# Performance work log

Hardware: AMD Instinct MI355X
Metric: run time of the kernel (lower is better)

The kernel has to match this reference:

```python
import jax, jax.numpy as jnp
import numpy as np

B, R, F = 64, 196, 2048   # batch, regions, feature_dim
E, H, A = 512, 512, 512   # embed_dim, hidden_dim, attn_dim
V, L = 12000, 24          # vocab, seq_len


def setup_inputs() -> dict:
    key = jax.random.key(0)
    ks = jax.random.split(key, 16)
    s = lambda *d: 1.0 / np.sqrt(d[-1])
    inp = {
        'image_feats': jax.random.normal(ks[0], (B, R, F), jnp.float32),
        'caption_in': jax.random.randint(ks[1], (B, L), 0, V, jnp.int64),
        'emb_table': jax.random.normal(ks[2], (V, E), jnp.float32) * 0.02,
        'W_init_h': jax.random.normal(ks[3], (H, F), jnp.float32) * s(F),
        'b_init_h': jnp.zeros((H,), jnp.float32),
        'W_init_c': jax.random.normal(ks[4], (H, F), jnp.float32) * s(F),
        'b_init_c': jnp.zeros((H,), jnp.float32),
        'W_ih': jax.random.normal(ks[5], (4 * H, E + F), jnp.float32) * s(E + F),
        'b_ih': jnp.zeros((4 * H,), jnp.float32),
        'W_hh': jax.random.normal(ks[6], (4 * H, H), jnp.float32) * s(H),
        'b_hh': jnp.zeros((4 * H,), jnp.float32),
        'W_featp': jax.random.normal(ks[7], (A, F), jnp.float32) * s(F),
        'b_featp': jnp.zeros((A,), jnp.float32),
        'W_hidp': jax.random.normal(ks[8], (A, H), jnp.float32) * s(H),
        'b_hidp': jnp.zeros((A,), jnp.float32),
        'W_score': jax.random.normal(ks[9], (1, A), jnp.float32) * s(A),
        'b_score': jnp.zeros((1,), jnp.float32),
        'W_out': jax.random.normal(ks[10], (V, H), jnp.float32) * s(H),
        'b_out': jnp.zeros((V,), jnp.float32),
    }
    return inp


def _forward(image_feats, caption_in, emb_table, W_init_h, b_init_h, W_init_c,
             b_init_c, W_ih, b_ih, W_hh, b_hh, W_featp, b_featp, W_hidp,
             b_hidp, W_score, b_score, W_out, b_out):
    # init hidden state from mean image features
    mean_feats = image_feats.mean(axis=1)                      # (B, F)
    h0 = mean_feats @ W_init_h.T + b_init_h                    # (B, H)
    c0 = mean_feats @ W_init_c.T + b_init_c                    # (B, H)

    embeddings = emb_table[caption_in]                         # (B, L, E)  (dropout in eval mode = identity)

    # feature projection is constant over timesteps -> hoist out of the scan
    feat_proj = jnp.einsum('brf,af->bra', image_feats, W_featp) + b_featp  # (B, R, A)

    def step(carry, emb_t):
        h, c = carry
        # additive attention
        hid_proj = h @ W_hidp.T + b_hidp                       # (B, A)
        energy = jnp.tanh(feat_proj + hid_proj[:, None, :])    # (B, R, A)
        scores = jnp.einsum('bra,a->br', energy, W_score[0]) + b_score[0]
        alpha = jax.nn.softmax(scores, axis=1)                 # (B, R)
        context = jnp.einsum('br,brf->bf', alpha, image_feats) # (B, F)
        # LSTM cell (PyTorch gate order: i, f, g, o)
        x = jnp.concatenate([emb_t, context], axis=1)          # (B, E+F)
        gates = x @ W_ih.T + b_ih + h @ W_hh.T + b_hh          # (B, 4H)
        i, f, g, o = jnp.split(gates, 4, axis=1)
        c_new = jax.nn.sigmoid(f) * c + jax.nn.sigmoid(i) * jnp.tanh(g)
        h_new = jax.nn.sigmoid(o) * jnp.tanh(c_new)
        out = h_new @ W_out.T + b_out                          # (B, V)
        return (h_new, c_new), (out, alpha)

    emb_t = jnp.swapaxes(embeddings, 0, 1)                     # (L, B, E)
    _, (preds, alphas) = jax.lax.scan(step, (h0, c0), emb_t)
    predictions = jnp.swapaxes(preds, 0, 1)                    # (B, L, V)
    all_alphas = jnp.swapaxes(alphas, 0, 1)                    # (B, L, R)
    return predictions, all_alphas


def reference(image_feats, caption_in, emb_table, W_init_h, b_init_h, W_init_c,
              b_init_c, W_ih, b_ih, W_hh, b_hh, W_featp, b_featp, W_hidp,
              b_hidp, W_score, b_score, W_out, b_out):
    return _forward(image_feats, caption_in, emb_table, W_init_h, b_init_h,
                    W_init_c, b_init_c, W_ih, b_ih, W_hh, b_hh, W_featp,
                    b_featp, W_hidp, b_hidp, W_score, b_score, W_out, b_out)
```

## Files before the change

kernel.cpp:

```cpp
#include <hip/hip_runtime.h>

#define B_ 64
#define R_ 196
#define F_ 2048
#define E_ 512
#define H_ 512
#define A_ 512
#define V_ 12000
#define L_ 24

typedef __attribute__((ext_vector_type(8))) short bf16x8;
typedef __attribute__((ext_vector_type(4))) float f32x4;
typedef unsigned short ush;

__device__ __forceinline__ float fast_tanh(float x) {
    float t = __expf(2.f * x);
    return 1.f - 2.f / (t + 1.f);
}
__device__ __forceinline__ float fast_sig(float x) {
    return 1.f / (1.f + __expf(-x));
}
__device__ __forceinline__ ush f2bf(float x) {
    unsigned int u = __float_as_uint(x);
    return (ush)((u + 0x7fffu + ((u >> 16) & 1u)) >> 16);
}
__device__ __forceinline__ float bf2f(ush b) {
    return __uint_as_float(((unsigned int)b) << 16);
}

#define LROW 40

template<int SPLIT, int CMAP, bool NFAST>
__global__ __launch_bounds__(512) void gemm_big128(
    const ush* __restrict__ Ah, const ush* __restrict__ Al, int lda,
    const ush* __restrict__ Wh, const ush* __restrict__ Wl, int ldw,
    const float* __restrict__ bias, void* __restrict__ Cv,
    int ldc, int N, int K)
{
    constexpr int SMEM_BYTES = (SPLIT == 3) ? 61440 : 30720;
    __shared__ __align__(16) char smem[SMEM_BYTES];
    ush* sAh = (ush*)smem;
    ush* sBh = (ush*)(smem + 10240);
    ush* sAl = (ush*)(smem + 30720);
    ush* sBl = (ush*)(smem + 40960);

    const int tid = threadIdx.x;
    const int lane = tid & 63, w = tid >> 6;
    const int mw = w >> 2, nw = w & 3;

    const int nbx = gridDim.x, nby = gridDim.y;
    const int nwg = nbx * nby;
    const int orig = blockIdx.x + nbx * blockIdx.y;
    const int q = nwg >> 3, r = nwg & 7;
    const int xcd = orig & 7, idx = orig >> 3;
    const int lin = (xcd < r ? xcd * (q + 1) : r * (q + 1) + (xcd - r) * q) + idx;
    int bx, by;
    if constexpr (NFAST) { by = lin % nby; bx = lin / nby; }
    else                 { bx = lin % nbx; by = lin / nbx; }
    const int mtile = bx * 128;
    const int ntile = by * 256;

    const int fr = lane & 15, kg = (lane >> 4) * 8;
    const int arow = tid >> 2, aq = (tid & 3) * 8;

    f32x4 acc[4][4];
    #pragma unroll
    for (int mf = 0; mf < 4; ++mf)
        #pragma unroll
        for (int nf = 0; nf < 4; ++nf) acc[mf][nf] = {0.f, 0.f, 0.f, 0.f};

    const uint4 zv = make_uint4(0u, 0u, 0u, 0u);

    for (int kb = 0; kb < K; kb += 32) {
        uint4 a_h = *(const uint4*)(Ah + (size_t)(mtile + arow) * lda + kb + aq);
        uint4 a_l;
        uint4 b_h[2], b_l[2];
        #pragma unroll
        for (int p = 0; p < 2; ++p) {
            const int row = ntile + arow + 128 * p;
            b_h[p] = (row < N) ? *(const uint4*)(Wh + (size_t)row * ldw + kb + aq) : zv;
        }
        if constexpr (SPLIT == 3) {
            a_l = *(const uint4*)(Al + (size_t)(mtile + arow) * lda + kb + aq);
            #pragma unroll
            for (int p = 0; p < 2; ++p) {
                const int row = ntile + arow + 128 * p;
                b_l[p] = (row < N) ? *(const uint4*)(Wl + (size_t)row * ldw + kb + aq) : zv;
            }
        }

        __syncthreads();
        *(uint4*)(sAh + arow * LROW + aq) = a_h;
        #pragma unroll
        for (int p = 0; p < 2; ++p)
            *(uint4*)(sBh + (arow + 128 * p) * LROW + aq) = b_h[p];
        if constexpr (SPLIT == 3) {
            *(uint4*)(sAl + arow * LROW + aq) = a_l;
            #pragma unroll
            for (int p = 0; p < 2; ++p)
                *(uint4*)(sBl + (arow + 128 * p) * LROW + aq) = b_l[p];
        }
        __syncthreads();

        bf16x8 bh[4], bl[4];
        #pragma unroll
        for (int nf = 0; nf < 4; ++nf) {
            bh[nf] = *(const bf16x8*)(sBh + (nw * 64 + nf * 16 + fr) * LROW + kg);
            if constexpr (SPLIT == 3)
                bl[nf] = *(const bf16x8*)(sBl + (nw * 64 + nf * 16 + fr) * LROW + kg);
        }
        #pragma unroll
        for (int mf = 0; mf < 4; ++mf) {
            const bf16x8 ah = *(const bf16x8*)(sAh + (mw * 64 + mf * 16 + fr) * LROW + kg);
            if constexpr (SPLIT == 3) {
                const bf16x8 al = *(const bf16x8*)(sAl + (mw * 64 + mf * 16 + fr) * LROW + kg);
                #pragma unroll
                for (int nf = 0; nf < 4; ++nf) {
                    acc[mf][nf] = __builtin_amdgcn_mfma_f32_16x16x32_bf16(ah, bh[nf], acc[mf][nf], 0, 0, 0);
                    acc[mf][nf] = __builtin_amdgcn_mfma_f32_16x16x32_bf16(ah, bl[nf], acc[mf][nf], 0, 0, 0);
                    acc[mf][nf] = __builtin_amdgcn_mfma_f32_16x16x32_bf16(al, bh[nf], acc[mf][nf], 0, 0, 0);
                }
            } else {
                #pragma unroll
                for (int nf = 0; nf < 4; ++nf)
                    acc[mf][nf] = __builtin_amdgcn_mfma_f32_16x16x32_bf16(ah, bh[nf], acc[mf][nf], 0, 0, 0);
            }
        }
    }

    #pragma unroll
    for (int nf = 0; nf < 4; ++nf) {
        const int nn = ntile + nw * 64 + nf * 16 + fr;
        if (nn < N) {
            const float bv = bias ? bias[nn] : 0.f;
            #pragma unroll
            for (int mf = 0; mf < 4; ++mf) {
                #pragma unroll
                for (int rr = 0; rr < 4; ++rr) {
                    const int m = mtile + mw * 64 + mf * 16 + (lane >> 4) * 4 + rr;
                    const float v = acc[mf][nf][rr] + bv;
                    if constexpr (CMAP == 1)
                        ((ush*)Cv)[(size_t)m * ldc + nn] = f2bf(v);
                    else if constexpr (CMAP == 2) {
                        float* dst = (float*)Cv + (size_t)(m & 63) * (L_ * V_)
                                   + (size_t)(m >> 6) * V_ + nn;
                        __builtin_nontemporal_store(v, dst);
                    } else
                        ((float*)Cv)[(size_t)m * ldc + nn] = v;
                }
            }
        }
    }
}

template<int SPLIT, int CMAP, bool NFAST>
__global__ __launch_bounds__(256) void gemm_big(
    const ush* __restrict__ Ah, const ush* __restrict__ Al, int lda,
    const ush* __restrict__ Wh, const ush* __restrict__ Wl, int ldw,
    const float* __restrict__ bias, void* __restrict__ Cv,
    int ldc, int N, int K)
{
    constexpr int SMEM_BYTES = (SPLIT == 3) ? 51200 : 25600;
    __shared__ __align__(16) char smem[SMEM_BYTES];
    ush* sAh = (ush*)smem;
    ush* sBh = (ush*)(smem + 5120);
    ush* sAl = (ush*)(smem + 25600);
    ush* sBl = (ush*)(smem + 30720);

    const int tid = threadIdx.x;
    const int lane = tid & 63, w = tid >> 6;

    const int nbx = gridDim.x, nby = gridDim.y;
    const int nwg = nbx * nby;
    int lin = blockIdx.x + nbx * blockIdx.y;
    if ((nwg & 7) == 0) {
        const int q = nwg >> 3;
        lin = (lin & 7) * q + (lin >> 3);
    }
    int bx, by;
    if constexpr (NFAST) { by = lin % nby; bx = lin / nby; }
    else                 { bx = lin % nbx; by = lin / nbx; }
    const int mtile = bx * 64;
    const int ntile = by * 256;

    const int fr = lane & 15, kg = (lane >> 4) * 8;
    const int arow = tid >> 2, aq = (tid & 3) * 8;

    f32x4 acc[4][4];
    #pragma unroll
    for (int mf = 0; mf < 4; ++mf)
        #pragma unroll
        for (int nf = 0; nf < 4; ++nf) acc[mf][nf] = {0.f, 0.f, 0.f, 0.f};

    const uint4 zv = make_uint4(0u, 0u, 0u, 0u);

    for (int kb = 0; kb < K; kb += 32) {
        uint4 a_h = *(const uint4*)(Ah + (size_t)(mtile + arow) * lda + kb + aq);
        uint4 a_l;
        uint4 b_h[4], b_l[4];
        #pragma unroll
        for (int p = 0; p < 4; ++p) {
            const int row = ntile + arow + 64 * p;
            b_h[p] = (row < N) ? *(const uint4*)(Wh + (size_t)row * ldw + kb + aq) : zv;
        }
        if constexpr (SPLIT == 3) {
            a_l = *(const uint4*)(Al + (size_t)(mtile + arow) * lda + kb + aq);
            #pragma unroll
            for (int p = 0; p < 4; ++p) {
                const int row = ntile + arow + 64 * p;
                b_l[p] = (row < N) ? *(const uint4*)(Wl + (size_t)row * ldw + kb + aq) : zv;
            }
        }

        __syncthreads();
        *(uint4*)(sAh + arow * LROW + aq) = a_h;
        #pragma unroll
        for (int p = 0; p < 4; ++p)
            *(uint4*)(sBh + (arow + 64 * p) * LROW + aq) = b_h[p];
        if constexpr (SPLIT == 3) {
            *(uint4*)(sAl + arow * LROW + aq) = a_l;
            #pragma unroll
            for (int p = 0; p < 4; ++p)
                *(uint4*)(sBl + (arow + 64 * p) * LROW + aq) = b_l[p];
        }
        __syncthreads();

        bf16x8 bh[4], bl[4];
        #pragma unroll
        for (int nf = 0; nf < 4; ++nf) {
            bh[nf] = *(const bf16x8*)(sBh + (w * 64 + nf * 16 + fr) * LROW + kg);
            if constexpr (SPLIT == 3)
                bl[nf] = *(const bf16x8*)(sBl + (w * 64 + nf * 16 + fr) * LROW + kg);
        }
        #pragma unroll
        for (int mf = 0; mf < 4; ++mf) {
            const bf16x8 ah = *(const bf16x8*)(sAh + (mf * 16 + fr) * LROW + kg);
            if constexpr (SPLIT == 3) {
                const bf16x8 al = *(const bf16x8*)(sAl + (mf * 16 + fr) * LROW + kg);
                #pragma unroll
                for (int nf = 0; nf < 4; ++nf) {
                    acc[mf][nf] = __builtin_amdgcn_mfma_f32_16x16x32_bf16(ah, bh[nf], acc[mf][nf], 0, 0, 0);
                    acc[mf][nf] = __builtin_amdgcn_mfma_f32_16x16x32_bf16(ah, bl[nf], acc[mf][nf], 0, 0, 0);
                    acc[mf][nf] = __builtin_amdgcn_mfma_f32_16x16x32_bf16(al, bh[nf], acc[mf][nf], 0, 0, 0);
                }
            } else {
                #pragma unroll
                for (int nf = 0; nf < 4; ++nf)
                    acc[mf][nf] = __builtin_amdgcn_mfma_f32_16x16x32_bf16(ah, bh[nf], acc[mf][nf], 0, 0, 0);
            }
        }
    }

    #pragma unroll
    for (int nf = 0; nf < 4; ++nf) {
        const int nn = ntile + w * 64 + nf * 16 + fr;
        if (nn < N) {
            const float bv = bias ? bias[nn] : 0.f;
            #pragma unroll
            for (int mf = 0; mf < 4; ++mf) {
                #pragma unroll
                for (int rr = 0; rr < 4; ++rr) {
                    const int m = mtile + mf * 16 + (lane >> 4) * 4 + rr;
                    const float v = acc[mf][nf][rr] + bv;
                    if constexpr (CMAP == 1)
                        ((ush*)Cv)[(size_t)m * ldc + nn] = f2bf(v);
                    else
                        ((float*)Cv)[(size_t)m * ldc + nn] = v;
                }
            }
        }
    }
}

__global__ __launch_bounds__(256) void gemm_gates(
    const ush* __restrict__ Ah0, const ush* __restrict__ Al0, int lda0, int k0,
    const ush* __restrict__ Ah1, const ush* __restrict__ Al1, int lda1,
    const ush* __restrict__ Wh, const ush* __restrict__ Wl, int ldw,
    float* __restrict__ C, int ldc, long zstride, int kChunk)
{
    __shared__ ush sAh[64 * LROW];
    __shared__ ush sBh[64 * LROW];
    __shared__ ush sAl[64 * LROW];
    __shared__ ush sBl[64 * LROW];

    const int tid = threadIdx.x;
    const int ntile = blockIdx.x * 64;
    const int kStart = blockIdx.z * kChunk;
    const int lane = tid & 63, w = tid >> 6;
    const int lrow = tid >> 2;
    const int lcol = (tid & 3) * 8;
    const int nrow = ntile + lrow;

    f32x4 acc[4];
    #pragma unroll
    for (int f = 0; f < 4; ++f) acc[f] = {0.f, 0.f, 0.f, 0.f};

    const int fr = lane & 15;
    const int kg = (lane >> 4) * 8;

    for (int kb = kStart; kb < kStart + kChunk; kb += 32) {
        const ush *ph, *pl; int lda, loc;
        if (kb < k0) { ph = Ah0; pl = Al0; lda = lda0; loc = kb; }
        else         { ph = Ah1; pl = Al1; lda = lda1; loc = kb - k0; }

        uint4 a_h = *(const uint4*)(ph + (size_t)lrow * lda + loc + lcol);
        uint4 b_h = *(const uint4*)(Wh + (size_t)nrow * ldw + kb + lcol);
        uint4 a_l = *(const uint4*)(pl + (size_t)lrow * lda + loc + lcol);
        uint4 b_l = *(const uint4*)(Wl + (size_t)nrow * ldw + kb + lcol);

        __syncthreads();
        *(uint4*)(sAh + lrow * LROW + lcol) = a_h;
        *(uint4*)(sBh + lrow * LROW + lcol) = b_h;
        *(uint4*)(sAl + lrow * LROW + lcol) = a_l;
        *(uint4*)(sBl + lrow * LROW + lcol) = b_l;
        __syncthreads();

        const bf16x8 bh = *(const bf16x8*)(sBh + (16 * w + fr) * LROW + kg);
        const bf16x8 bl = *(const bf16x8*)(sBl + (16 * w + fr) * LROW + kg);

        #pragma unroll
        for (int f = 0; f < 4; ++f) {
            const bf16x8 ah = *(const bf16x8*)(sAh + (16 * f + fr) * LROW + kg);
            const bf16x8 al = *(const bf16x8*)(sAl + (16 * f + fr) * LROW + kg);
            acc[f] = __builtin_amdgcn_mfma_f32_16x16x32_bf16(ah, bh, acc[f], 0, 0, 0);
            acc[f] = __builtin_amdgcn_mfma_f32_16x16x32_bf16(ah, bl, acc[f], 0, 0, 0);
            acc[f] = __builtin_amdgcn_mfma_f32_16x16x32_bf16(al, bh, acc[f], 0, 0, 0);
        }
    }

    const int n = ntile + 16 * w + (lane & 15);
    float* Cz = C + (size_t)blockIdx.z * zstride;
    #pragma unroll
    for (int f = 0; f < 4; ++f)
        #pragma unroll
        for (int rr = 0; rr < 4; ++rr) {
            const int m = 16 * f + (lane >> 4) * 4 + rr;
            Cz[(size_t)m * ldc + n] = acc[f][rr];
        }
}

__global__ __launch_bounds__(256) void prep_feats(
    const float* __restrict__ feats, ush* __restrict__ fbh,
    ush* __restrict__ mh, ush* __restrict__ ml)
{
    const int fs = blockIdx.x;
    const int b  = blockIdx.y;
    const int f = fs * 512 + threadIdx.x * 2;
    const float2* fp = (const float2*)(feats + (size_t)b * R_ * F_ + f);
    ush* fo = fbh + (size_t)b * R_ * F_ + f;
    float sx = 0.f, sy = 0.f;
    for (int r = 0; r < R_; ++r) {
        const float2 v = fp[(size_t)r * (F_ / 2)];
        sx += v.x; sy += v.y;
        ushort2 u; u.x = f2bf(v.x); u.y = f2bf(v.y);
        *(ushort2*)(fo + (size_t)r * F_) = u;
    }
    const float s = 1.f / (float)R_;
    sx *= s; sy *= s;
    const size_t mi = (size_t)b * F_ + f;
    const ush hx = f2bf(sx); mh[mi] = hx;     ml[mi] = f2bf(sx - bf2f(hx));
    const ush hy = f2bf(sy); mh[mi + 1] = hy; ml[mi + 1] = f2bf(sy - bf2f(hy));
}

__global__ __launch_bounds__(256) void gather_split(
    const float* __restrict__ emb, const int* __restrict__ cap,
    ush* __restrict__ eh, ush* __restrict__ el)
{
    const int idx = blockIdx.x * 256 + threadIdx.x;
    const int bt = idx >> 7, j = idx & 127;
    const int tok = cap[bt];
    const float4 v = reinterpret_cast<const float4*>(emb)[(size_t)tok * (E_ / 4) + j];
    const float a[4] = {v.x, v.y, v.z, v.w};
    #pragma unroll
    for (int c = 0; c < 4; ++c) {
        const ush hi = f2bf(a[c]);
        eh[idx * 4 + c] = hi;
        el[idx * 4 + c] = f2bf(a[c] - bf2f(hi));
    }
}

__global__ __launch_bounds__(256) void split_kernel(
    const float* __restrict__ in, ush* __restrict__ hi, ush* __restrict__ lo, int n4)
{
    for (int i = blockIdx.x * 256 + threadIdx.x; i < n4; i += gridDim.x * 256) {
        const float4 v = reinterpret_cast<const float4*>(in)[i];
        const float a[4] = {v.x, v.y, v.z, v.w};
        #pragma unroll
        for (int c = 0; c < 4; ++c) {
            const ush h = f2bf(a[c]);
            hi[i * 4 + c] = h;
            if (lo) lo[i * 4 + c] = f2bf(a[c] - bf2f(h));
        }
    }
}

__global__ __launch_bounds__(256) void prep_wih(
    const float* __restrict__ W_ih, const float* __restrict__ W_hh,
    ush* __restrict__ wxh, ush* __restrict__ wxl,
    ush* __restrict__ wg2h, ush* __restrict__ wg2l)
{
    const int nrow = blockIdx.x;
    for (int k = threadIdx.x; k < E_; k += 256) {
        const float v = W_ih[(size_t)nrow * (E_ + F_) + k];
        const ush h = f2bf(v);
        wxh[(size_t)nrow * E_ + k] = h;
        wxl[(size_t)nrow * E_ + k] = f2bf(v - bf2f(h));
    }
    for (int k = threadIdx.x; k < F_ + H_; k += 256) {
        const float v = (k < F_) ? W_ih[(size_t)nrow * (E_ + F_) + E_ + k]
                                 : W_hh[(size_t)nrow * H_ + (k - F_)];
        const ush h = f2bf(v);
        wg2h[(size_t)nrow * (F_ + H_) + k] = h;
        wg2l[(size_t)nrow * (F_ + H_) + k] = f2bf(v - bf2f(h));
    }
}

__global__ __launch_bounds__(256) void transpose512(
    const float* __restrict__ in, float* __restrict__ out)
{
    const int idx = blockIdx.x * 256 + threadIdx.x;
    const int k = idx >> 9, a = idx & 511;
    out[idx] = in[(size_t)a * 512 + k];
    (void)k;
}

__global__ __launch_bounds__(256) void init_reduce(
    const float* __restrict__ initp, const float* __restrict__ b_init_h,
    const float* __restrict__ b_init_c, float* __restrict__ h0f,
    float* __restrict__ c, ush* __restrict__ h_hi, ush* __restrict__ h_lo)
{
    const int idx = blockIdx.x * 256 + threadIdx.x;
    const int b = idx >> 10, n = idx & 1023;
    float s = 0.f;
    #pragma unroll
    for (int z = 0; z < 8; ++z)
        s += initp[(size_t)z * (B_ * 1024) + (size_t)b * 1024 + n];
    if (n < 512) {
        s += b_init_h[n];
        h0f[b * H_ + n] = s;
        const ush hi = f2bf(s);
        h_hi[b * H_ + n] = hi;
        h_lo[b * H_ + n] = f2bf(s - bf2f(hi));
    } else {
        s += b_init_c[n - 512];
        c[b * H_ + (n - 512)] = s;
    }
}

template<bool ATT>
__global__ __launch_bounds__(512) void step_kernel(
    const float* __restrict__ gparts, const float* __restrict__ egates,
    const float* __restrict__ b_ih, const float* __restrict__ b_hh,
    float* __restrict__ c, const float* __restrict__ h0f,
    ush* __restrict__ h_hi, ush* __restrict__ h_lo,
    ush* __restrict__ hall_hi, ush* __restrict__ hall_lo,
    const float* __restrict__ whpT, const float* __restrict__ b_hidp,
    const ush* __restrict__ fpb, const float* __restrict__ W_score,
    const float* __restrict__ b_score,
    float* __restrict__ alpha, float* __restrict__ alph_out, int t)
{
    __shared__ float sh_h[H_];
    __shared__ float sh_hp[A_];
    __shared__ float sh_ws[A_];
    __shared__ float sh_sc[200];
    __shared__ float red[2];
    const int tid = threadIdx.x;
    const int b = blockIdx.x;
    const int n = tid;

    float hh;
    if (t > 0) {
        const float* eg = egates + ((size_t)b * L_ + (t - 1)) * 2048;
        float gi = b_ih[n] + b_hh[n] + eg[n];
        float gf = b_ih[n + 512] + b_hh[n + 512] + eg[n + 512];
        float gg = b_ih[n + 1024] + b_hh[n + 1024] + eg[n + 1024];
        float go = b_ih[n + 1536] + b_hh[n + 1536] + eg[n + 1536];
        #pragma unroll
        for (int z = 0; z < 8; ++z) {
            const float* gz = gparts + (size_t)z * B_ * 2048 + (size_t)b * 2048;
            gi += gz[n]; gf += gz[n + 512]; gg += gz[n + 1024]; go += gz[n + 1536];
        }
        const float cc = fast_sig(gf) * c[b * H_ + n] + fast_sig(gi) * fast_tanh(gg);
        hh = fast_sig(go) * fast_tanh(cc);
        c[b * H_ + n] = cc;
        const ush hi = f2bf(hh);
        const ush lo = f2bf(hh - bf2f(hi));
        h_hi[b * H_ + n] = hi;
        h_lo[b * H_ + n] = lo;
        const size_t hidx = ((size_t)(t - 1) * B_ + b) * H_ + n;
        hall_hi[hidx] = hi;
        hall_lo[hidx] = lo;
    } else {
        hh = h0f[b * H_ + n];
    }
    if constexpr (!ATT) return;

    sh_h[n] = hh;
    sh_ws[n] = W_score[n];
    __syncthreads();

    {
        float a0 = 0.f, a1 = 0.f, a2 = 0.f, a3 = 0.f;
        #pragma unroll 4
        for (int k = 0; k < H_; k += 4) {
            a0 = fmaf(sh_h[k + 0], whpT[(size_t)(k + 0) * A_ + tid], a0);
            a1 = fmaf(sh_h[k + 1], whpT[(size_t)(k + 1) * A_ + tid], a1);
            a2 = fmaf(sh_h[k + 2], whpT[(size_t)(k + 2) * A_ + tid], a2);
            a3 = fmaf(sh_h[k + 3], whpT[(size_t)(k + 3) * A_ + tid], a3);
        }
        sh_hp[tid] = (a0 + a1) + (a2 + a3) + b_hidp[tid];
    }
    __syncthreads();

    const int lane = tid & 63, wid = tid >> 6;
    for (int r = wid; r < R_; r += 8) {
        const ushort2* row = reinterpret_cast<const ushort2*>(fpb + ((size_t)b * R_ + r) * A_);
        float acc = 0.f;
        #pragma unroll
        for (int j = 0; j < 4; ++j) {
            const ushort2 u = row[lane + 64 * j];
            const int a = 2 * (lane + 64 * j);
            acc += fast_tanh(bf2f(u.x) + sh_hp[a]) * sh_ws[a];
            acc += fast_tanh(bf2f(u.y) + sh_hp[a + 1]) * sh_ws[a + 1];
        }
        for (int off = 32; off > 0; off >>= 1) acc += __shfl_down(acc, off);
        if (lane == 0) sh_sc[r] = acc + b_score[0];
    }
    __syncthreads();

    if (tid < 64) {
        float m = -1e30f;
        for (int r = tid; r < R_; r += 64) m = fmaxf(m, sh_sc[r]);
        for (int off = 32; off > 0; off >>= 1) m = fmaxf(m, __shfl_xor(m, off));
        float s = 0.f;
        for (int r = tid; r < R_; r += 64) s += __expf(sh_sc[r] - m);
        for (int off = 32; off > 0; off >>= 1) s += __shfl_xor(s, off);
        if (tid == 0) { red[0] = m; red[1] = 1.f / s; }
    }
    __syncthreads();
    const float m = red[0], is = red[1];
    if (tid < R_) {
        const float av = __expf(sh_sc[tid] - m) * is;
        alpha[b * R_ + tid] = av;
        alph_out[((size_t)b * L_ + t) * R_ + tid] = av;
    }
}

__global__ __launch_bounds__(256) void ctx_kernel(
    const ush* __restrict__ fbh, const float* __restrict__ alpha,
    ush* __restrict__ ctx_hi, ush* __restrict__ ctx_lo)
{
    __shared__ float sa[R_];
    const int tid = threadIdx.x;
    const int fs = blockIdx.x;
    const int b = blockIdx.y;
    if (tid < R_) sa[tid] = alpha[b * R_ + tid];
    __syncthreads();

    const int f0 = fs * 512 + tid * 2;
    const ush* fp = fbh + (size_t)b * R_ * F_ + f0;
    float cx = 0.f, cy = 0.f;
    #pragma unroll 4
    for (int r = 0; r < R_; ++r) {
        const float a = sa[r];
        const ushort2 u = *(const ushort2*)(fp + (size_t)r * F_);
        cx = fmaf(a, bf2f(u.x), cx); cy = fmaf(a, bf2f(u.y), cy);
    }
    const size_t ci = (size_t)b * F_ + f0;
    const ush hx = f2bf(cx);
    ctx_hi[ci] = hx; ctx_lo[ci] = f2bf(cx - bf2f(hx));
    const ush hy = f2bf(cy);
    ctx_hi[ci + 1] = hy; ctx_lo[ci + 1] = f2bf(cy - bf2f(hy));
}

extern "C" void kernel_launch(void* const* d_in, const int* in_sizes, int n_in,
                              void* d_out, int out_size, void* d_ws, size_t ws_size,
                              hipStream_t stream)
{
    const float* feats    = (const float*)d_in[0];
    const int*   cap      = (const int*)  d_in[1];
    const float* emb      = (const float*)d_in[2];
    const float* W_init_h = (const float*)d_in[3];
    const float* b_init_h = (const float*)d_in[4];
    const float* W_init_c = (const float*)d_in[5];
    const float* b_init_c = (const float*)d_in[6];
    const float* W_ih     = (const float*)d_in[7];
    const float* b_ih     = (const float*)d_in[8];
    const float* W_hh     = (const float*)d_in[9];
    const float* b_hh     = (const float*)d_in[10];
    const float* W_featp  = (const float*)d_in[11];
    const float* b_featp  = (const float*)d_in[12];
    const float* W_hidp   = (const float*)d_in[13];
    const float* b_hidp   = (const float*)d_in[14];
    const float* W_score  = (const float*)d_in[15];
    const float* b_score  = (const float*)d_in[16];
    const float* W_out    = (const float*)d_in[17];
    const float* b_out    = (const float*)d_in[18];

    float* pred     = (float*)d_out;
    float* alph_out = pred + (size_t)B_ * L_ * V_;

    char* p = (char*)d_ws;
    auto alloc = [&](size_t bytes) { char* q = p; p += (bytes + 255) & ~(size_t)255; return q; };

    ush*   fpb    = (ush*)  alloc((size_t)B_ * R_ * A_ * 2);
    ush*   eh     = (ush*)  alloc((size_t)B_ * L_ * E_ * 2);
    ush*   el     = (ush*)  alloc((size_t)B_ * L_ * E_ * 2);
    ush*   mh     = (ush*)  alloc((size_t)B_ * F_ * 2);
    ush*   ml     = (ush*)  alloc((size_t)B_ * F_ * 2);
    ush*   fbh    = (ush*)  alloc((size_t)B_ * R_ * F_ * 2);
    ush*   wfp_h  = (ush*)  alloc((size_t)A_ * F_ * 2);
    ush*   wiH    = (ush*)  alloc((size_t)1024 * F_ * 2);
    ush*   wiL    = (ush*)  alloc((size_t)1024 * F_ * 2);
    ush*   wxh    = (ush*)  alloc((size_t)2048 * E_ * 2);
    ush*   wxl    = (ush*)  alloc((size_t)2048 * E_ * 2);
    ush*   wg2h   = (ush*)  alloc((size_t)2048 * (F_ + H_) * 2);
    ush*   wg2l   = (ush*)  alloc((size_t)2048 * (F_ + H_) * 2);
    ush*   woh    = (ush*)  alloc((size_t)V_ * H_ * 2);
    ush*   wol    = (ush*)  alloc((size_t)V_ * H_ * 2);
    float* whpT   = (float*)alloc((size_t)H_ * A_ * 4);
    float* egates = (float*)alloc((size_t)B_ * L_ * 2048 * 4);
    float* h0f    = (float*)alloc((size_t)B_ * H_ * 4);
    float* c      = (float*)alloc((size_t)B_ * H_ * 4);
    ush*   h_hi   = (ush*)  alloc((size_t)B_ * H_ * 2);
    ush*   h_lo   = (ush*)  alloc((size_t)B_ * H_ * 2);
    ush*   hallh  = (ush*)  alloc((size_t)L_ * B_ * H_ * 2);
    ush*   halll  = (ush*)  alloc((size_t)L_ * B_ * H_ * 2);
    ush*   ctx_hi = (ush*)  alloc((size_t)B_ * F_ * 2);
    ush*   ctx_lo = (ush*)  alloc((size_t)B_ * F_ * 2);
    float* alpha  = (float*)alloc((size_t)B_ * R_ * 4);
    float* gparts = (float*)alloc((size_t)8 * B_ * 2048 * 4);
    float* initp  = (float*)alloc((size_t)8 * B_ * 1024 * 4);

    prep_feats<<<dim3(4, B_), 256, 0, stream>>>(feats, fbh, mh, ml);
    gather_split<<<768, 256, 0, stream>>>(emb, cap, eh, el);
    split_kernel<<<2048, 256, 0, stream>>>(W_out, woh, wol, V_ * H_ / 4);
    split_kernel<<<512, 256, 0, stream>>>(W_init_h, wiH, wiL, H_ * F_ / 4);
    split_kernel<<<512, 256, 0, stream>>>(W_init_c, wiH + (size_t)512 * F_,
                                          wiL + (size_t)512 * F_, H_ * F_ / 4);
    split_kernel<<<512, 256, 0, stream>>>(W_featp, wfp_h, nullptr, A_ * F_ / 4);
    prep_wih<<<2048, 256, 0, stream>>>(W_ih, W_hh, wxh, wxl, wg2h, wg2l);
    transpose512<<<1024, 256, 0, stream>>>(W_hidp, whpT);

    gemm_gates<<<dim3(16, 1, 8), 256, 0, stream>>>(
        mh, ml, F_, F_,
        mh, ml, F_,
        wiH, wiL, F_,
        initp, 1024, (long)B_ * 1024, F_ / 8);
    init_reduce<<<256, 256, 0, stream>>>(initp, b_init_h, b_init_c, h0f, c, h_hi, h_lo);

    gemm_big128<1, 1, true><<<dim3(98, 2), 512, 0, stream>>>(
        fbh, nullptr, F_, wfp_h, nullptr, F_, b_featp, fpb, A_, A_, F_);

    gemm_big<3, 0, false><<<dim3(24, 8), 256, 0, stream>>>(
        eh, el, E_, wxh, wxl, E_, nullptr, egates, 2048, 2048, E_);

    for (int t = 0; t < L_; ++t) {
        step_kernel<true><<<B_, 512, 0, stream>>>(
            gparts, egates, b_ih, b_hh, c, h0f, h_hi, h_lo, hallh, halll,
            whpT, b_hidp, fpb, W_score, b_score, alpha, alph_out, t);

        ctx_kernel<<<dim3(4, B_), 256, 0, stream>>>(fbh, alpha, ctx_hi, ctx_lo);

        gemm_gates<<<dim3(32, 1, 8), 256, 0, stream>>>(
            ctx_hi, ctx_lo, F_, F_,
            h_hi, h_lo, H_,
            wg2h, wg2l, F_ + H_,
            gparts, 4 * H_, (long)B_ * 4 * H_, (F_ + H_) / 8);
    }

    step_kernel<false><<<B_, 512, 0, stream>>>(
        gparts, egates, b_ih, b_hh, c, h0f, h_hi, h_lo, hallh, halll,
        whpT, b_hidp, fpb, W_score, b_score, alpha, alph_out, L_);

    gemm_big128<3, 2, false><<<dim3(12, 47), 512, 0, stream>>>(
        hallh, halll, H_, woh, wol, H_, b_out, pred, 0, V_, H_);
}
```

Before: 2.046 ms.

## Fuse attention context reduction into step kernel and retile feature projection

```diff
diff --git a/kernel.cpp b/kernel.cpp
--- a/kernel.cpp
+++ b/kernel.cpp
@@ -456,8 +456,9 @@
     ush* __restrict__ hall_hi, ush* __restrict__ hall_lo,
     const float* __restrict__ whpT, const float* __restrict__ b_hidp,
     const ush* __restrict__ fpb, const float* __restrict__ W_score,
-    const float* __restrict__ b_score,
-    float* __restrict__ alpha, float* __restrict__ alph_out, int t)
+    const float* __restrict__ b_score, const ush* __restrict__ fbh,
+    ush* __restrict__ ctx_hi, ush* __restrict__ ctx_lo,
+    float* __restrict__ alph_out, int t)
 {
     __shared__ float sh_h[H_];
     __shared__ float sh_hp[A_];
@@ -541,36 +542,33 @@
     const float m = red[0], is = red[1];
     if (tid < R_) {
         const float av = __expf(sh_sc[tid] - m) * is;
-        alpha[b * R_ + tid] = av;
+        sh_sc[tid] = av;
         alph_out[((size_t)b * L_ + t) * R_ + tid] = av;
     }
-}
-
-__global__ __launch_bounds__(256) void ctx_kernel(
-    const ush* __restrict__ fbh, const float* __restrict__ alpha,
-    ush* __restrict__ ctx_hi, ush* __restrict__ ctx_lo)
-{
-    __shared__ float sa[R_];
-    const int tid = threadIdx.x;
-    const int fs = blockIdx.x;
-    const int b = blockIdx.y;
-    if (tid < R_) sa[tid] = alpha[b * R_ + tid];
     __syncthreads();
 
-    const int f0 = fs * 512 + tid * 2;
-    const ush* fp = fbh + (size_t)b * R_ * F_ + f0;
-    float cx = 0.f, cy = 0.f;
-    #pragma unroll 4
-    for (int r = 0; r < R_; ++r) {
-        const float a = sa[r];
-        const ushort2 u = *(const ushort2*)(fp + (size_t)r * F_);
-        cx = fmaf(a, bf2f(u.x), cx); cy = fmaf(a, bf2f(u.y), cy);
-    }
-    const size_t ci = (size_t)b * F_ + f0;
-    const ush hx = f2bf(cx);
-    ctx_hi[ci] = hx; ctx_lo[ci] = f2bf(cx - bf2f(hx));
-    const ush hy = f2bf(cy);
-    ctx_hi[ci + 1] = hy; ctx_lo[ci + 1] = f2bf(cy - bf2f(hy));
+    {
+        const int f0 = tid << 2;
+        const ush* fp2 = fbh + (size_t)b * R_ * F_ + f0;
+        float c0 = 0.f, c1 = 0.f, c2 = 0.f, c3 = 0.f;
+        #pragma unroll 2
+        for (int r = 0; r < R_; ++r) {
+            const float a = sh_sc[r];
+            const ushort4 u = *(const ushort4*)(fp2 + (size_t)r * F_);
+            c0 = fmaf(a, bf2f(u.x), c0);
+            c1 = fmaf(a, bf2f(u.y), c1);
+            c2 = fmaf(a, bf2f(u.z), c2);
+            c3 = fmaf(a, bf2f(u.w), c3);
+        }
+        ushort4 hi4, lo4;
+        hi4.x = f2bf(c0); lo4.x = f2bf(c0 - bf2f(hi4.x));
+        hi4.y = f2bf(c1); lo4.y = f2bf(c1 - bf2f(hi4.y));
+        hi4.z = f2bf(c2); lo4.z = f2bf(c2 - bf2f(hi4.z));
+        hi4.w = f2bf(c3); lo4.w = f2bf(c3 - bf2f(hi4.w));
+        const size_t ci = (size_t)b * F_ + f0;
+        *(ushort4*)(ctx_hi + ci) = hi4;
+        *(ushort4*)(ctx_lo + ci) = lo4;
+    }
 }
 
 extern "C" void kernel_launch(void* const* d_in, const int* in_sizes, int n_in,
@@ -628,7 +626,6 @@
     ush*   halll  = (ush*)  alloc((size_t)L_ * B_ * H_ * 2);
     ush*   ctx_hi = (ush*)  alloc((size_t)B_ * F_ * 2);
     ush*   ctx_lo = (ush*)  alloc((size_t)B_ * F_ * 2);
-    float* alpha  = (float*)alloc((size_t)B_ * R_ * 4);
     float* gparts = (float*)alloc((size_t)8 * B_ * 2048 * 4);
     float* initp  = (float*)alloc((size_t)8 * B_ * 1024 * 4);
 
@@ -649,7 +646,7 @@
         initp, 1024, (long)B_ * 1024, F_ / 8);
     init_reduce<<<256, 256, 0, stream>>>(initp, b_init_h, b_init_c, h0f, c, h_hi, h_lo);
 
-    gemm_big128<1, 1, true><<<dim3(98, 2), 512, 0, stream>>>(
+    gemm_big<1, 1, true><<<dim3(196, 2), 256, 0, stream>>>(
         fbh, nullptr, F_, wfp_h, nullptr, F_, b_featp, fpb, A_, A_, F_);
 
     gemm_big<3, 0, false><<<dim3(24, 8), 256, 0, stream>>>(
@@ -658,9 +655,8 @@
     for (int t = 0; t < L_; ++t) {
         step_kernel<true><<<B_, 512, 0, stream>>>(
             gparts, egates, b_ih, b_hh, c, h0f, h_hi, h_lo, hallh, halll,
-            whpT, b_hidp, fpb, W_score, b_score, alpha, alph_out, t);
-
-        ctx_kernel<<<dim3(4, B_), 256, 0, stream>>>(fbh, alpha, ctx_hi, ctx_lo);
+            whpT, b_hidp, fpb, W_score, b_score, fbh, ctx_hi, ctx_lo,
+            alph_out, t);
 
         gemm_gates<<<dim3(32, 1, 8), 256, 0, stream>>>(
             ctx_hi, ctx_lo, F_, F_,
@@ -671,7 +667,8 @@
 
     step_kernel<false><<<B_, 512, 0, stream>>>(
         gparts, egates, b_ih, b_hh, c, h0f, h_hi, h_lo, hallh, halll,
-        whpT, b_hidp, fpb, W_score, b_score, alpha, alph_out, L_);
+        whpT, b_hidp, fpb, W_score, b_score, fbh, ctx_hi, ctx_lo,
+        alph_out, L_);
 
     gemm_big128<3, 2, false><<<dim3(12, 47), 512, 0, stream>>>(
         hallh, halll, H_, woh, wol, H_, b_out, pred, 0, V_, H_);
```

After: 2.309 ms. 1.13x slower.
